# Performance work log

Hardware: AMD Instinct MI355X
Metric: run time of the kernel (lower is better)

The kernel has to match this reference:

```python
import jax, jax.numpy as jnp
import numpy as np

N_HEADS = 64 * 4 // 32  # 8 heads, head_dim 32
LN_EPS = 1e-5


def conv3d(x, w, b):
    # x: [B,C,D,H,W], w: [O,I,3,3,3], padding=1 == SAME for k=3
    y = jax.lax.conv_general_dilated(
        x, w, window_strides=(1, 1, 1), padding='SAME',
        dimension_numbers=('NCDHW', 'OIDHW', 'NCDHW'))
    return y + b[None, :, None, None, None]


def layer_norm(x, g, b):
    m = jnp.mean(x, axis=-1, keepdims=True)
    v = jnp.var(x, axis=-1, keepdims=True)  # biased var, as torch LayerNorm
    return (x - m) * jax.lax.rsqrt(v + LN_EPS) * g + b


def linear(x, w, b):
    # torch Linear layout: w [out, in]
    return jnp.einsum('bsi,oi->bso', x, w) + b


def setup_inputs() -> dict:
    key = jax.random.key(0)
    ks = jax.random.split(key, 16)
    C_in, d = 64, 256
    x = jax.random.normal(ks[0], (1, C_in, 16, 16, 16), dtype=jnp.float32)
    s = 0.02
    params = {
        'conv1_w': jax.random.normal(ks[1], (d, C_in, 3, 3, 3), jnp.float32) * s,
        'conv1_b': jnp.zeros((d,), jnp.float32),
        'ln_g': jnp.ones((d,), jnp.float32),
        'ln_b': jnp.zeros((d,), jnp.float32),
        'q_w': jax.random.normal(ks[2], (d, d), jnp.float32) * s,
        'q_b': jnp.zeros((d,), jnp.float32),
        'k_w': jax.random.normal(ks[3], (d, d), jnp.float32) * s,
        'k_b': jnp.zeros((d,), jnp.float32),
        'v_w': jax.random.normal(ks[4], (d, d), jnp.float32) * s,
        'v_b': jnp.zeros((d,), jnp.float32),
        'ffn_w': jax.random.normal(ks[5], (d, d), jnp.float32) * s,
        'ffn_b': jnp.zeros((d,), jnp.float32),
        'conv2_w': jax.random.normal(ks[6], (C_in, d, 3, 3, 3), jnp.float32) * s,
        'conv2_b': jnp.zeros((C_in,), jnp.float32),
    }
    return {'x': x, **params}


def reference(x, conv1_w, conv1_b, ln_g, ln_b, q_w, q_b, k_w, k_b, v_w, v_b,
              ffn_w, ffn_b, conv2_w, conv2_b):
    B, _, D, H, W = x.shape
    S = D * H * W
    # PositionalEmbedding: conv3d then flatten; the learned pos-emb is a
    # freshly-initialized zeros Parameter in the original => no-op add.
    h0 = conv3d(x, conv1_w, conv1_b)              # [B, d, D, H, W]
    d_model = h0.shape[1]
    h0 = h0.reshape(B, d_model, S).transpose(0, 2, 1)  # [B, S, d]

    hn = layer_norm(h0, ln_g, ln_b)
    hd = d_model // N_HEADS

    def split_heads(t):
        return t.reshape(B, S, N_HEADS, hd).transpose(0, 2, 1, 3)  # [B, nH, S, hd]

    q = split_heads(linear(hn, q_w, q_b))
    k = split_heads(linear(hn, k_w, k_b))
    v = split_heads(linear(hn, v_w, v_b))

    scores = jnp.einsum('bhqd,bhkd->bhqk', q, k) / jnp.sqrt(
        jnp.asarray(hd, q.dtype))
    # NOTE: original uses nn.Softmax(dim=2) -> normalize over QUERY axis
    attn = jax.nn.softmax(scores, axis=2)
    out = jnp.einsum('bhqk,bhkd->bhqd', attn, v)  # [B, nH, S, hd]
    out = out.transpose(0, 2, 1, 3).reshape(B, S, d_model)

    xt = out + hn                                  # residual onto NORMED input
    h2 = layer_norm(xt, ln_g, ln_b)                # same LN weights reused
    h3 = jax.nn.relu(linear(h2, ffn_w, ffn_b)) + xt

    h3 = h3.transpose(0, 2, 1).reshape(B, d_model, D, H, W)
    return conv3d(h3, conv2_w, conv2_b)
```

## Files before the change

### kernel.cpp

```cpp
#include <hip/hip_runtime.h>
#include <math.h>

#define S 4096
#define DM 256

using short8 = __attribute__((ext_vector_type(8))) short;
using short4v = __attribute__((ext_vector_type(4))) short;
using f32x4 = __attribute__((ext_vector_type(4))) float;
using f32x16 = __attribute__((ext_vector_type(16))) float;

static constexpr float QK_SCALE_LOG2E = 0.17677669529663687f * 1.4426950408889634f;

__device__ __forceinline__ short f2bf(float f) {
  union { float f; unsigned u; } v;
  v.f = f;
  unsigned r = (v.u + 0x7FFFu + ((v.u >> 16) & 1u)) >> 16;
  return (short)r;
}

__device__ __forceinline__ float bf2f(short s) {
  union { unsigned u; float f; } v;
  v.u = ((unsigned)(unsigned short)s) << 16;
  return v.f;
}

__device__ __forceinline__ unsigned cvt_pk_bf16(float lo, float hi) {
  unsigned r;
  asm("v_cvt_pk_bf16_f32 %0, %1, %2" : "=v"(r) : "v"(lo), "v"(hi));
  return r;
}

__device__ __forceinline__ float fexp2(float x) {
  float r;
  asm("v_exp_f32 %0, %1" : "=v"(r) : "v"(x));
  return r;
}

__device__ __forceinline__ int pad_idx(int s) {
  int d = s >> 8, h = (s >> 4) & 15, w = s & 15;
  return ((d + 1) * 18 + (h + 1)) * 18 + (w + 1);
}

__global__ __launch_bounds__(256) void k_prep(const float* __restrict__ x,
                                              const float* __restrict__ c1w,
                                              const float* __restrict__ c2w,
                                              const float* __restrict__ qw,
                                              const float* __restrict__ kw,
                                              const float* __restrict__ vw,
                                              const float* __restrict__ fw,
                                              short* __restrict__ xpad,
                                              short* __restrict__ w1t,
                                              short* __restrict__ w2t,
                                              short* __restrict__ wqkvf,
                                              short* __restrict__ hpad) {
  int bid = blockIdx.x, tid = threadIdx.x;
  if (bid < 1458) {
    int idx = bid * 256 + tid;
    int row = idx >> 6, c = idx & 63;
    int pd = row / 324, rem = row - pd * 324;
    int ph = rem / 18, pw = rem - ph * 18;
    short v = 0;
    if ((unsigned)(pd - 1) < 16u && (unsigned)(ph - 1) < 16u && (unsigned)(pw - 1) < 16u) {
      int s = (pd - 1) * 256 + (ph - 1) * 16 + (pw - 1);
      v = f2bf(x[c * 4096 + s]);
    }
    xpad[idx] = v;
  } else if (bid < 3186) {
    int idx = (bid - 1458) * 256 + tid;
    int o = idx / 1728, r = idx - o * 1728;
    int off = r >> 6, ic = r & 63;
    w1t[idx] = f2bf(c1w[(o * 64 + ic) * 27 + off]);
  } else if (bid < 4914) {
    int idx = (bid - 3186) * 256 + tid;
    int o = idx / 6912, r = idx - o * 6912;
    int off = r >> 8, ic = r & 255;
    w2t[idx] = f2bf(c2w[(o * 256 + ic) * 27 + off]);
  } else if (bid < 5938) {
    int idx = (bid - 4914) * 256 + tid;
    int which = idx >> 16, r = idx & 65535;
    const float* src = (which == 0) ? qw : (which == 1) ? kw : (which == 2) ? vw : fw;
    wqkvf[idx] = f2bf(src[r]);
  } else {
    int i = (bid - 5938) * 2048 + tid * 8;
    short8 z = {0, 0, 0, 0, 0, 0, 0, 0};
    *(short8*)(hpad + i) = z;
  }
}

__global__ __launch_bounds__(256) void k_conv1m(const short* __restrict__ xpad,
                                                const short* __restrict__ wt,
                                                const float* __restrict__ bias,
                                                float* __restrict__ h0) {
  int bid = blockIdx.x;
  int mt = bid >> 1, ch = bid & 1;
  int tid = threadIdx.x, w = tid >> 6, lane = tid & 63, g = lane >> 4, c = lane & 15;
  int d = mt >> 4, h = mt & 15;
  int nb = ch * 128 + w * 32;
  f32x4 acc0 = {0.f, 0.f, 0.f, 0.f}, acc1 = {0.f, 0.f, 0.f, 0.f};
  for (int off = 0; off < 27; ++off) {
    int kd = off / 9, r = off - kd * 9, kh = r / 3, kw = r - kh * 3;
    int rowb = ((d + kd) * 18 + h + kh) * 18 + kw + c;
#pragma unroll
    for (int kc = 0; kc < 2; ++kc) {
      short8 af = *(const short8*)(xpad + rowb * 64 + kc * 32 + 8 * g);
      int kidx = off * 64 + kc * 32 + 8 * g;
      short8 b0 = *(const short8*)(wt + (nb + c) * 1728 + kidx);
      short8 b1 = *(const short8*)(wt + (nb + 16 + c) * 1728 + kidx);
      acc0 = __builtin_amdgcn_mfma_f32_16x16x32_bf16(af, b0, acc0, 0, 0, 0);
      acc1 = __builtin_amdgcn_mfma_f32_16x16x32_bf16(af, b1, acc1, 0, 0, 0);
    }
  }
  int o0 = nb + c, o1 = nb + 16 + c;
  float bv0 = bias[o0], bv1 = bias[o1];
#pragma unroll
  for (int i = 0; i < 4; ++i) {
    int s = mt * 16 + 4 * g + i;
    h0[s * 256 + o0] = acc0[i] + bv0;
    h0[s * 256 + o1] = acc1[i] + bv1;
  }
}

__global__ __launch_bounds__(256) void k_layernorm(const float* __restrict__ in,
                                                   const float* __restrict__ g,
                                                   const float* __restrict__ b,
                                                   float* __restrict__ outf,
                                                   short* __restrict__ outb) {
  int s = blockIdx.x, tid = threadIdx.x;
  float xv = in[s * 256 + tid];
  float s1 = xv, s2 = xv * xv;
#pragma unroll
  for (int off = 32; off > 0; off >>= 1) {
    s1 += __shfl_down(s1, off);
    s2 += __shfl_down(s2, off);
  }
  __shared__ float w1[4], w2[4], mb[2];
  int wid = tid >> 6;
  if ((tid & 63) == 0) { w1[wid] = s1; w2[wid] = s2; }
  __syncthreads();
  if (tid == 0) {
    float t1 = w1[0] + w1[1] + w1[2] + w1[3];
    float t2 = w2[0] + w2[1] + w2[2] + w2[3];
    float m = t1 * (1.f / 256.f);
    float var = t2 * (1.f / 256.f) - m * m;
    mb[0] = m;
    mb[1] = rsqrtf(var + 1e-5f);
  }
  __syncthreads();
  float y = (xv - mb[0]) * mb[1] * g[tid] + b[tid];
  outf[s * 256 + tid] = y;
  outb[s * 256 + tid] = f2bf(y);
}

__global__ __launch_bounds__(256) void k_gemm_qkv(const short* __restrict__ ab,
                                                  const short* __restrict__ wqb,
                                                  const short* __restrict__ wkb,
                                                  const short* __restrict__ wvb,
                                                  const float* __restrict__ qbi,
                                                  const float* __restrict__ kbi,
                                                  const float* __restrict__ vbi,
                                                  short* __restrict__ qb,
                                                  short* __restrict__ kb,
                                                  short* __restrict__ vt) {
  int y = blockIdx.y;
  const short* wb = (y == 0) ? wqb : ((y == 1) ? wkb : wvb);
  int tid = threadIdx.x, w = tid >> 6, lane = tid & 63, g = lane >> 4, c = lane & 15;
  int m0 = blockIdx.x * 16;
  int nb = w * 64;
  f32x4 acc[4];
#pragma unroll
  for (int n = 0; n < 4; ++n) acc[n] = {0.f, 0.f, 0.f, 0.f};
#pragma unroll 2
  for (int k0 = 0; k0 < 256; k0 += 32) {
    short8 af = *(const short8*)(ab + (m0 + c) * 256 + k0 + 8 * g);
#pragma unroll
    for (int n = 0; n < 4; ++n) {
      short8 bf = *(const short8*)(wb + (nb + 16 * n + c) * 256 + k0 + 8 * g);
      acc[n] = __builtin_amdgcn_mfma_f32_16x16x32_bf16(af, bf, acc[n], 0, 0, 0);
    }
  }
  if (y < 2) {
    const float* bi = (y == 0) ? qbi : kbi;
    float sc = (y == 0) ? QK_SCALE_LOG2E : 1.f;
    short* ob = (y == 0) ? qb : kb;
#pragma unroll
    for (int n = 0; n < 4; ++n) {
      int o = nb + 16 * n + c;
      float bv = bi[o];
      int hh = o >> 5, dj = o & 31;
#pragma unroll
      for (int i = 0; i < 4; ++i) {
        int s = m0 + 4 * g + i;
        ob[((size_t)hh * S + s) * 32 + dj] = f2bf((acc[n][i] + bv) * sc);
      }
    }
  } else {
#pragma unroll
    for (int n = 0; n < 4; ++n) {
      int o = nb + 16 * n + c;
      float bv = vbi[o];
      short4v st;
#pragma unroll
      for (int i = 0; i < 4; ++i) st[i] = f2bf(acc[n][i] + bv);
      *(short4v*)(vt + (size_t)o * S + m0 + 4 * g) = st;
    }
  }
}

__global__ __launch_bounds__(256) void k_attn1(const short* __restrict__ qb,
                                               const short* __restrict__ kb,
                                               float* __restrict__ lpart) {
  int b = blockIdx.x;
  int qs = b & 7, kt = (b >> 3) & 31, h = b >> 8;
  int tid = threadIdx.x;
  int w = tid >> 6, lane = tid & 63;
  int lo = lane & 31, hi = lane >> 5;
  int k0 = kt * 128 + w * 32;
  const size_t hb = (size_t)h * S;
  const short* krow = kb + (hb + k0 + lo) * 32;
  short8 ak0 = *(const short8*)(krow + 8 * hi);
  short8 ak1 = *(const short8*)(krow + 16 + 8 * hi);
  f32x16 ls = {};
  const f32x16 z16 = {};
  int qend = qs * 512 + 512;
  for (int q0 = qs * 512; q0 < qend; q0 += 32) {
    short8 bq0 = *(const short8*)(qb + (hb + q0 + lo) * 32 + 8 * hi);
    short8 bq1 = *(const short8*)(qb + (hb + q0 + lo) * 32 + 16 + 8 * hi);
    __builtin_amdgcn_s_setprio(1);
    f32x16 p = __builtin_amdgcn_mfma_f32_32x32x16_bf16(ak0, bq0, z16, 0, 0, 0);
    p = __builtin_amdgcn_mfma_f32_32x32x16_bf16(ak1, bq1, p, 0, 0, 0);
    __builtin_amdgcn_s_setprio(0);
#pragma unroll
    for (int r = 0; r < 16; ++r) ls[r] += fexp2(p[r]);
  }
#pragma unroll
  for (int r = 0; r < 16; ++r) {
    float v = ls[r];
    v += __shfl_xor(v, 1);
    v += __shfl_xor(v, 2);
    v += __shfl_xor(v, 4);
    v += __shfl_xor(v, 8);
    v += __shfl_xor(v, 16);
    ls[r] = v;
  }
  if (lo == 0) {
#pragma unroll
    for (int r = 0; r < 16; ++r)
      lpart[qs * 32768 + h * 4096 + k0 + (r & 3) + 8 * (r >> 2) + 4 * hi] = ls[r];
  }
}

__global__ __launch_bounds__(256) void k_scalevt(short* __restrict__ vt,
                                                 const float* __restrict__ lpart) {
  int idx = blockIdx.x * 256 + threadIdx.x;
  int row = idx >> 9;
  int col0 = (idx & 511) << 3;
  int h = row >> 5;
  const float* lp = lpart + h * 4096 + col0;
  float4 s0 = {0.f, 0.f, 0.f, 0.f}, s1 = {0.f, 0.f, 0.f, 0.f};
#pragma unroll
  for (int j = 0; j < 8; ++j) {
    float4 a = *(const float4*)(lp + j * 32768);
    float4 b = *(const float4*)(lp + j * 32768 + 4);
    s0.x += a.x; s0.y += a.y; s0.z += a.z; s0.w += a.w;
    s1.x += b.x; s1.y += b.y; s1.z += b.z; s1.w += b.w;
  }
  float4 l0, l1;
  l0.x = 1.f / s0.x; l0.y = 1.f / s0.y; l0.z = 1.f / s0.z; l0.w = 1.f / s0.w;
  l1.x = 1.f / s1.x; l1.y = 1.f / s1.y; l1.z = 1.f / s1.z; l1.w = 1.f / s1.w;
  short8 v = *(short8*)(vt + (size_t)row * S + col0);
  union { unsigned u[4]; short8 s8; } r;
  r.u[0] = cvt_pk_bf16(bf2f(v[0]) * l0.x, bf2f(v[1]) * l0.y);
  r.u[1] = cvt_pk_bf16(bf2f(v[2]) * l0.z, bf2f(v[3]) * l0.w);
  r.u[2] = cvt_pk_bf16(bf2f(v[4]) * l1.x, bf2f(v[5]) * l1.y);
  r.u[3] = cvt_pk_bf16(bf2f(v[6]) * l1.z, bf2f(v[7]) * l1.w);
  *(short8*)(vt + (size_t)row * S + col0) = r.s8;
}

__global__ __launch_bounds__(256, 4) void k_attn2(const short* __restrict__ qb,
                                                  const short* __restrict__ kb,
                                                  const short* __restrict__ vt,
                                                  short* __restrict__ parts) {
  int b = blockIdx.x;
  int ks = b & 7, qt = (b >> 3) & 15, h = b >> 7;
  int tid = threadIdx.x;
  int w = tid >> 6, lane = tid & 63;
  int lo = lane & 31, hi = lane >> 5;
  int sl = lo ^ ((((lo >> 2) ^ (lo >> 3)) & 1) * 12);
  int q0a = qt * 256 + w * 64;
  int q0b = q0a + 32;
  const size_t hb = (size_t)h * S;
  short8 bqa0 = *(const short8*)(qb + (hb + q0a + lo) * 32 + 8 * hi);
  short8 bqa1 = *(const short8*)(qb + (hb + q0a + lo) * 32 + 16 + 8 * hi);
  short8 bqb0 = *(const short8*)(qb + (hb + q0b + lo) * 32 + 8 * hi);
  short8 bqb1 = *(const short8*)(qb + (hb + q0b + lo) * 32 + 16 + 8 * hi);
  f32x16 accA = {}, accB = {};
  const short* krow = kb + (hb + sl) * 32;
  const short* vrow = vt + ((size_t)(h * 32) + lo) * S;
  const f32x16 z16 = {};
  int k0 = ks * 512;
  short8 ak0 = *(const short8*)(krow + (size_t)k0 * 32 + 8 * hi);
  short8 ak1 = *(const short8*)(krow + (size_t)k0 * 32 + 16 + 8 * hi);
#pragma unroll 1
  for (int it = 0; it < 16; ++it) {
    int kn = k0 + 32;
    short8 nak0 = *(const short8*)(krow + (size_t)kn * 32 + 8 * hi);
    short8 nak1 = *(const short8*)(krow + (size_t)kn * 32 + 16 + 8 * hi);
    short8 bv0 = *(const short8*)(vrow + k0 + 8 * hi);
    short8 bv1 = *(const short8*)(vrow + k0 + 16 + 8 * hi);
    __builtin_amdgcn_s_setprio(1);
    f32x16 pA = __builtin_amdgcn_mfma_f32_32x32x16_bf16(ak0, bqa0, z16, 0, 0, 0);
    f32x16 pB = __builtin_amdgcn_mfma_f32_32x32x16_bf16(ak0, bqb0, z16, 0, 0, 0);
    pA = __builtin_amdgcn_mfma_f32_32x32x16_bf16(ak1, bqa1, pA, 0, 0, 0);
    pB = __builtin_amdgcn_mfma_f32_32x32x16_bf16(ak1, bqb1, pB, 0, 0, 0);
    __builtin_amdgcn_s_setprio(0);
    union { unsigned u[4]; short8 s8; } fA0, fA1, fB0, fB1;
#pragma unroll
    for (int m = 0; m < 4; ++m)
      fA0.u[m] = cvt_pk_bf16(fexp2(pA[2 * m]), fexp2(pA[2 * m + 1]));
#pragma unroll
    for (int m = 0; m < 4; ++m)
      fA1.u[m] = cvt_pk_bf16(fexp2(pA[8 + 2 * m]), fexp2(pA[9 + 2 * m]));
#pragma unroll
    for (int m = 0; m < 4; ++m)
      fB0.u[m] = cvt_pk_bf16(fexp2(pB[2 * m]), fexp2(pB[2 * m + 1]));
#pragma unroll
    for (int m = 0; m < 4; ++m)
      fB1.u[m] = cvt_pk_bf16(fexp2(pB[8 + 2 * m]), fexp2(pB[9 + 2 * m]));
    __builtin_amdgcn_s_setprio(1);
    accA = __builtin_amdgcn_mfma_f32_32x32x16_bf16(fA0.s8, bv0, accA, 0, 0, 0);
    accB = __builtin_amdgcn_mfma_f32_32x32x16_bf16(fB0.s8, bv0, accB, 0, 0, 0);
    accA = __builtin_amdgcn_mfma_f32_32x32x16_bf16(fA1.s8, bv1, accA, 0, 0, 0);
    accB = __builtin_amdgcn_mfma_f32_32x32x16_bf16(fB1.s8, bv1, accB, 0, 0, 0);
    __builtin_amdgcn_s_setprio(0);
    ak0 = nak0;
    ak1 = nak1;
    k0 = kn;
  }
  short* part = parts + (size_t)ks * (S * DM);
  int col = h * 32 + lo;
#pragma unroll
  for (int r = 0; r < 16; ++r) {
    int qrel = (r & 3) + 8 * (r >> 2) + 4 * hi;
    part[(q0a + qrel) * 256 + col] = f2bf(accA[r]);
    part[(q0b + qrel) * 256 + col] = f2bf(accB[r]);
  }
}

__global__ __launch_bounds__(256) void k_combine_ln(const short* __restrict__ parts,
                                                    const float* __restrict__ hn,
                                                    const float* __restrict__ g,
                                                    const float* __restrict__ b,
                                                    float* __restrict__ xt,
                                                    short* __restrict__ h2b) {
  int s = blockIdx.x, tid = threadIdx.x;
  int i = s * 256 + tid;
  const int SD4 = S * DM;
  float xv = hn[i];
#pragma unroll
  for (int j = 0; j < 8; ++j) xv += bf2f(parts[i + j * SD4]);
  xt[i] = xv;
  float s1 = xv, s2 = xv * xv;
#pragma unroll
  for (int off = 32; off > 0; off >>= 1) {
    s1 += __shfl_down(s1, off);
    s2 += __shfl_down(s2, off);
  }
  __shared__ float w1[4], w2[4], mb[2];
  int wid = tid >> 6;
  if ((tid & 63) == 0) { w1[wid] = s1; w2[wid] = s2; }
  __syncthreads();
  if (tid == 0) {
    float t1 = w1[0] + w1[1] + w1[2] + w1[3];
    float t2 = w2[0] + w2[1] + w2[2] + w2[3];
    float m = t1 * (1.f / 256.f);
    float var = t2 * (1.f / 256.f) - m * m;
    mb[0] = m;
    mb[1] = rsqrtf(var + 1e-5f);
  }
  __syncthreads();
  h2b[i] = f2bf((xv - mb[0]) * mb[1] * g[tid] + b[tid]);
}

__global__ __launch_bounds__(256) void k_gemm_ffn(const short* __restrict__ ab,
                                                  const short* __restrict__ wb,
                                                  const float* __restrict__ bi,
                                                  const float* __restrict__ xt,
                                                  short* __restrict__ hpad) {
  int tid = threadIdx.x, w = tid >> 6, lane = tid & 63, g = lane >> 4, c = lane & 15;
  int m0 = blockIdx.x * 16;
  int nb = w * 64;
  f32x4 acc[4];
#pragma unroll
  for (int n = 0; n < 4; ++n) acc[n] = {0.f, 0.f, 0.f, 0.f};
#pragma unroll 2
  for (int k0 = 0; k0 < 256; k0 += 32) {
    short8 af = *(const short8*)(ab + (m0 + c) * 256 + k0 + 8 * g);
#pragma unroll
    for (int n = 0; n < 4; ++n) {
      short8 bf = *(const short8*)(wb + (nb + 16 * n + c) * 256 + k0 + 8 * g);
      acc[n] = __builtin_amdgcn_mfma_f32_16x16x32_bf16(af, bf, acc[n], 0, 0, 0);
    }
  }
  int pr[4];
#pragma unroll
  for (int i = 0; i < 4; ++i) pr[i] = pad_idx(m0 + 4 * g + i) * 256;
#pragma unroll
  for (int n = 0; n < 4; ++n) {
    int o = nb + 16 * n + c;
    float bv = bi[o];
#pragma unroll
    for (int i = 0; i < 4; ++i) {
      int s = m0 + 4 * g + i;
      float v = acc[n][i] + bv;
      v = v > 0.f ? v : 0.f;
      hpad[pr[i] + o] = f2bf(v + xt[s * 256 + o]);
    }
  }
}

__global__ __launch_bounds__(256) void k_conv2m(const short* __restrict__ hpad,
                                                const short* __restrict__ wt,
                                                float* __restrict__ pbase) {
  __shared__ float red[3][16][65];
  int bid = blockIdx.x;
  int mt = bid >> 2, kh = bid & 3;
  int tid = threadIdx.x, w = tid >> 6, lane = tid & 63, g = lane >> 4, c = lane & 15;
  int d = mt >> 4, h = mt & 15;
  f32x4 acc[4];
#pragma unroll
  for (int n = 0; n < 4; ++n) acc[n] = {0.f, 0.f, 0.f, 0.f};
  int off0 = kh * 7;
  int offn = (kh == 3) ? 6 : 7;
  for (int off = off0 + w; off < off0 + offn; off += 4) {
    int kd = off / 9, rr = off - kd * 9, kkh = rr / 3, kw = rr - kkh * 3;
    int rowb = ((d + kd) * 18 + h + kkh) * 18 + kw + c;
    const short* arow = hpad + rowb * 256;
    const short* wrow = wt + off * 256;
#pragma unroll 2
    for (int kc = 0; kc < 8; ++kc) {
      short8 af = *(const short8*)(arow + kc * 32 + 8 * g);
#pragma unroll
      for (int n = 0; n < 4; ++n) {
        short8 bf = *(const short8*)(wrow + (16 * n + c) * 6912 + kc * 32 + 8 * g);
        acc[n] = __builtin_amdgcn_mfma_f32_16x16x32_bf16(af, bf, acc[n], 0, 0, 0);
      }
    }
  }
  if (w > 0) {
#pragma unroll
    for (int n = 0; n < 4; ++n)
#pragma unroll
      for (int i = 0; i < 4; ++i) red[w - 1][n * 4 + i][lane] = acc[n][i];
  }
  __syncthreads();
  if (w == 0) {
    float* pbuf = pbase + (size_t)kh * (S * DM / 4);
#pragma unroll
    for (int n = 0; n < 4; ++n) {
      int o = 16 * n + c;
      float4 st;
      st.x = acc[n][0] + red[0][n * 4 + 0][lane] + red[1][n * 4 + 0][lane] + red[2][n * 4 + 0][lane];
      st.y = acc[n][1] + red[0][n * 4 + 1][lane] + red[1][n * 4 + 1][lane] + red[2][n * 4 + 1][lane];
      st.z = acc[n][2] + red[0][n * 4 + 2][lane] + red[1][n * 4 + 2][lane] + red[2][n * 4 + 2][lane];
      st.w = acc[n][3] + red[0][n * 4 + 3][lane] + red[1][n * 4 + 3][lane] + red[2][n * 4 + 3][lane];
      *(float4*)(pbuf + o * 4096 + mt * 16 + 4 * g) = st;
    }
  }
}

__global__ __launch_bounds__(256) void k_conv2fin(const float* __restrict__ pbase,
                                                  const float* __restrict__ bias,
                                                  float* __restrict__ out) {
  int idx4 = (blockIdx.x * 256 + threadIdx.x) * 4;
  int o = idx4 >> 12;
  const int PS = S * DM / 4;
  float4 a = *(const float4*)(pbase + idx4);
  float4 b = *(const float4*)(pbase + PS + idx4);
  float4 c = *(const float4*)(pbase + 2 * PS + idx4);
  float4 d = *(const float4*)(pbase + 3 * PS + idx4);
  float bv = bias[o];
  float4 r;
  r.x = a.x + b.x + c.x + d.x + bv;
  r.y = a.y + b.y + c.y + d.y + bv;
  r.z = a.z + b.z + c.z + d.z + bv;
  r.w = a.w + b.w + c.w + d.w + bv;
  *(float4*)(out + idx4) = r;
}

extern "C" void kernel_launch(void* const* d_in, const int* in_sizes, int n_in,
                              void* d_out, int out_size, void* d_ws, size_t ws_size,
                              hipStream_t stream) {
  const float* x   = (const float*)d_in[0];
  const float* c1w = (const float*)d_in[1];
  const float* c1b = (const float*)d_in[2];
  const float* lng = (const float*)d_in[3];
  const float* lnb = (const float*)d_in[4];
  const float* qw  = (const float*)d_in[5];
  const float* qbi = (const float*)d_in[6];
  const float* kw  = (const float*)d_in[7];
  const float* kbi = (const float*)d_in[8];
  const float* vw  = (const float*)d_in[9];
  const float* vbi = (const float*)d_in[10];
  const float* fw  = (const float*)d_in[11];
  const float* fbi = (const float*)d_in[12];
  const float* c2w = (const float*)d_in[13];
  const float* c2b = (const float*)d_in[14];
  float* out = (float*)d_out;
  float* ws = (float*)d_ws;

  const size_t SD = (size_t)S * DM;
  float* hn     = ws;
  float* xt     = hn + SD;
  short* partsb = (short*)(xt + SD);
  float* h0     = (float*)partsb;
  float* c2p    = (float*)partsb;
  float* lpart  = (float*)(partsb + 8 * SD);
  float* linv   = lpart + 262144;
  short* hnb    = (short*)(linv + 32768);
  short* h2b    = hnb + SD;
  short* qb     = h2b + SD;
  short* kb     = qb + SD;
  short* vt     = kb + SD;
  short* xpad   = vt + SD;
  short* hpad   = xpad + 373248;
  short* w1t    = hpad + 1492992;
  short* w2t    = w1t + 442368;
  short* wqb    = w2t + 442368;
  short* wkb    = wqb + 65536;
  short* wvb    = wkb + 65536;
  short* wfb    = wvb + 65536;

  k_prep<<<6667, 256, 0, stream>>>(x, c1w, c2w, qw, kw, vw, fw,
                                   xpad, w1t, w2t, wqb, hpad);

  k_conv1m<<<512, 256, 0, stream>>>(xpad, w1t, c1b, h0);
  k_layernorm<<<4096, 256, 0, stream>>>(h0, lng, lnb, hn, hnb);

  k_gemm_qkv<<<dim3(256, 3), 256, 0, stream>>>(hnb, wqb, wkb, wvb, qbi, kbi, vbi,
                                               qb, kb, vt);

  k_attn1<<<2048, 256, 0, stream>>>(qb, kb, lpart);
  k_scalevt<<<1024, 256, 0, stream>>>(vt, lpart);
  k_attn2<<<1024, 256, 0, stream>>>(qb, kb, vt, partsb);
  k_combine_ln<<<4096, 256, 0, stream>>>(partsb, hn, lng, lnb, xt, h2b);

  k_gemm_ffn<<<256, 256, 0, stream>>>(h2b, wfb, fbi, xt, hpad);
  k_conv2m<<<1024, 256, 0, stream>>>(hpad, w2t, c2p);
  k_conv2fin<<<256, 256, 0, stream>>>(c2p, c2b, out);
}
```

Baseline: 175.6 us.

## Process two spatial rows per block in convs to reuse weight fragments

```diff
diff --git a/kernel.cpp b/kernel.cpp
--- a/kernel.cpp
+++ b/kernel.cpp
@@ -92,31 +92,36 @@
                                                 const float* __restrict__ bias,
                                                 float* __restrict__ h0) {
   int bid = blockIdx.x;
-  int mt = bid >> 1, ch = bid & 1;
+  int mt2 = bid >> 1, ch = bid & 1;
   int tid = threadIdx.x, w = tid >> 6, lane = tid & 63, g = lane >> 4, c = lane & 15;
-  int d = mt >> 4, h = mt & 15;
+  int d = mt2 >> 3, h = (mt2 & 7) * 2;
   int nb = ch * 128 + w * 32;
-  f32x4 acc0 = {0.f, 0.f, 0.f, 0.f}, acc1 = {0.f, 0.f, 0.f, 0.f};
+  f32x4 accA0 = {}, accA1 = {}, accB0 = {}, accB1 = {};
   for (int off = 0; off < 27; ++off) {
     int kd = off / 9, r = off - kd * 9, kh = r / 3, kw = r - kh * 3;
     int rowb = ((d + kd) * 18 + h + kh) * 18 + kw + c;
 #pragma unroll
     for (int kc = 0; kc < 2; ++kc) {
-      short8 af = *(const short8*)(xpad + rowb * 64 + kc * 32 + 8 * g);
+      short8 afA = *(const short8*)(xpad + rowb * 64 + kc * 32 + 8 * g);
+      short8 afB = *(const short8*)(xpad + (rowb + 18) * 64 + kc * 32 + 8 * g);
       int kidx = off * 64 + kc * 32 + 8 * g;
       short8 b0 = *(const short8*)(wt + (nb + c) * 1728 + kidx);
       short8 b1 = *(const short8*)(wt + (nb + 16 + c) * 1728 + kidx);
-      acc0 = __builtin_amdgcn_mfma_f32_16x16x32_bf16(af, b0, acc0, 0, 0, 0);
-      acc1 = __builtin_amdgcn_mfma_f32_16x16x32_bf16(af, b1, acc1, 0, 0, 0);
+      accA0 = __builtin_amdgcn_mfma_f32_16x16x32_bf16(afA, b0, accA0, 0, 0, 0);
+      accA1 = __builtin_amdgcn_mfma_f32_16x16x32_bf16(afA, b1, accA1, 0, 0, 0);
+      accB0 = __builtin_amdgcn_mfma_f32_16x16x32_bf16(afB, b0, accB0, 0, 0, 0);
+      accB1 = __builtin_amdgcn_mfma_f32_16x16x32_bf16(afB, b1, accB1, 0, 0, 0);
     }
   }
   int o0 = nb + c, o1 = nb + 16 + c;
   float bv0 = bias[o0], bv1 = bias[o1];
+  int sA = mt2 * 32 + 4 * g;
 #pragma unroll
   for (int i = 0; i < 4; ++i) {
-    int s = mt * 16 + 4 * g + i;
-    h0[s * 256 + o0] = acc0[i] + bv0;
-    h0[s * 256 + o1] = acc1[i] + bv1;
+    h0[(sA + i) * 256 + o0] = accA0[i] + bv0;
+    h0[(sA + i) * 256 + o1] = accA1[i] + bv1;
+    h0[(sA + 16 + i) * 256 + o0] = accB0[i] + bv0;
+    h0[(sA + 16 + i) * 256 + o1] = accB1[i] + bv1;
   }
 }
 
@@ -209,8 +214,10 @@
 __global__ __launch_bounds__(256) void k_attn1(const short* __restrict__ qb,
                                                const short* __restrict__ kb,
                                                float* __restrict__ lpart) {
-  int b = blockIdx.x;
-  int qs = b & 7, kt = (b >> 3) & 31, h = b >> 8;
+  int bid = blockIdx.x;
+  int h = bid & 7;
+  int rest = bid >> 3;
+  int kt = rest >> 3, qs = rest & 7;
   int tid = threadIdx.x;
   int w = tid >> 6, lane = tid & 63;
   int lo = lane & 31, hi = lane >> 5;
@@ -280,8 +287,10 @@
                                                   const short* __restrict__ kb,
                                                   const short* __restrict__ vt,
                                                   short* __restrict__ parts) {
-  int b = blockIdx.x;
-  int ks = b & 7, qt = (b >> 3) & 15, h = b >> 7;
+  int bid = blockIdx.x;
+  int h = bid & 7;
+  int rest = bid >> 3;
+  int qt = rest >> 3, ks = rest & 7;
   int tid = threadIdx.x;
   int w = tid >> 6, lane = tid & 63;
   int lo = lane & 31, hi = lane >> 5;
@@ -421,28 +430,31 @@
 __global__ __launch_bounds__(256) void k_conv2m(const short* __restrict__ hpad,
                                                 const short* __restrict__ wt,
                                                 float* __restrict__ pbase) {
-  __shared__ float red[3][16][65];
+  __shared__ float red[3][32][65];
   int bid = blockIdx.x;
-  int mt = bid >> 2, kh = bid & 3;
+  int mt2 = bid >> 2, kh = bid & 3;
   int tid = threadIdx.x, w = tid >> 6, lane = tid & 63, g = lane >> 4, c = lane & 15;
-  int d = mt >> 4, h = mt & 15;
-  f32x4 acc[4];
-#pragma unroll
-  for (int n = 0; n < 4; ++n) acc[n] = {0.f, 0.f, 0.f, 0.f};
+  int d = mt2 >> 3, h = (mt2 & 7) * 2;
+  f32x4 accA[4], accB[4];
+#pragma unroll
+  for (int n = 0; n < 4; ++n) { accA[n] = {0.f, 0.f, 0.f, 0.f}; accB[n] = {0.f, 0.f, 0.f, 0.f}; }
   int off0 = kh * 7;
   int offn = (kh == 3) ? 6 : 7;
   for (int off = off0 + w; off < off0 + offn; off += 4) {
     int kd = off / 9, rr = off - kd * 9, kkh = rr / 3, kw = rr - kkh * 3;
     int rowb = ((d + kd) * 18 + h + kkh) * 18 + kw + c;
-    const short* arow = hpad + rowb * 256;
+    const short* arowA = hpad + rowb * 256;
+    const short* arowB = hpad + (rowb + 18) * 256;
     const short* wrow = wt + off * 256;
 #pragma unroll 2
     for (int kc = 0; kc < 8; ++kc) {
-      short8 af = *(const short8*)(arow + kc * 32 + 8 * g);
+      short8 afA = *(const short8*)(arowA + kc * 32 + 8 * g);
+      short8 afB = *(const short8*)(arowB + kc * 32 + 8 * g);
 #pragma unroll
       for (int n = 0; n < 4; ++n) {
         short8 bf = *(const short8*)(wrow + (16 * n + c) * 6912 + kc * 32 + 8 * g);
-        acc[n] = __builtin_amdgcn_mfma_f32_16x16x32_bf16(af, bf, acc[n], 0, 0, 0);
+        accA[n] = __builtin_amdgcn_mfma_f32_16x16x32_bf16(afA, bf, accA[n], 0, 0, 0);
+        accB[n] = __builtin_amdgcn_mfma_f32_16x16x32_bf16(afB, bf, accB[n], 0, 0, 0);
       }
     }
   }
@@ -450,7 +462,10 @@
 #pragma unroll
     for (int n = 0; n < 4; ++n)
 #pragma unroll
-      for (int i = 0; i < 4; ++i) red[w - 1][n * 4 + i][lane] = acc[n][i];
+      for (int i = 0; i < 4; ++i) {
+        red[w - 1][n * 4 + i][lane] = accA[n][i];
+        red[w - 1][16 + n * 4 + i][lane] = accB[n][i];
+      }
   }
   __syncthreads();
   if (w == 0) {
@@ -458,12 +473,16 @@
 #pragma unroll
     for (int n = 0; n < 4; ++n) {
       int o = 16 * n + c;
-      float4 st;
-      st.x = acc[n][0] + red[0][n * 4 + 0][lane] + red[1][n * 4 + 0][lane] + red[2][n * 4 + 0][lane];
-      st.y = acc[n][1] + red[0][n * 4 + 1][lane] + red[1][n * 4 + 1][lane] + red[2][n * 4 + 1][lane];
-      st.z = acc[n][2] + red[0][n * 4 + 2][lane] + red[1][n * 4 + 2][lane] + red[2][n * 4 + 2][lane];
-      st.w = acc[n][3] + red[0][n * 4 + 3][lane] + red[1][n * 4 + 3][lane] + red[2][n * 4 + 3][lane];
-      *(float4*)(pbuf + o * 4096 + mt * 16 + 4 * g) = st;
+      float4 stA, stB;
+#pragma unroll
+      for (int i = 0; i < 4; ++i) {
+        float a = accA[n][i] + red[0][n * 4 + i][lane] + red[1][n * 4 + i][lane] + red[2][n * 4 + i][lane];
+        float bb = accB[n][i] + red[0][16 + n * 4 + i][lane] + red[1][16 + n * 4 + i][lane] + red[2][16 + n * 4 + i][lane];
+        ((float*)&stA)[i] = a;
+        ((float*)&stB)[i] = bb;
+      }
+      *(float4*)(pbuf + o * 4096 + mt2 * 32 + 4 * g) = stA;
+      *(float4*)(pbuf + o * 4096 + mt2 * 32 + 16 + 4 * g) = stB;
     }
   }
 }
@@ -533,7 +552,7 @@
   k_prep<<<6667, 256, 0, stream>>>(x, c1w, c2w, qw, kw, vw, fw,
                                    xpad, w1t, w2t, wqb, hpad);
 
-  k_conv1m<<<512, 256, 0, stream>>>(xpad, w1t, c1b, h0);
+  k_conv1m<<<256, 256, 0, stream>>>(xpad, w1t, c1b, h0);
   k_layernorm<<<4096, 256, 0, stream>>>(h0, lng, lnb, hn, hnb);
 
   k_gemm_qkv<<<dim3(256, 3), 256, 0, stream>>>(hnb, wqb, wkb, wvb, qbi, kbi, vbi,
@@ -545,6 +564,6 @@
   k_combine_ln<<<4096, 256, 0, stream>>>(partsb, hn, lng, lnb, xt, h2b);
 
   k_gemm_ffn<<<256, 256, 0, stream>>>(h2b, wfb, fbi, xt, hpad);
-  k_conv2m<<<1024, 256, 0, stream>>>(hpad, w2t, c2p);
+  k_conv2m<<<512, 256, 0, stream>>>(hpad, w2t, c2p);
   k_conv2fin<<<256, 256, 0, stream>>>(c2p, c2b, out);
 }
```

New measurement: 151.0 us. 14.0% less time.
